# Kernel tuning notes

Hardware: AMD Instinct MI355X
Metric: run time of the kernel (lower is better)

## Reference

```python
import jax, jax.numpy as jnp
import numpy as np

B, T, N, F_DIM = 8, 32, 64, 6
D, H, C = 128, 4, 32          # hidden, spatial heads, head dim
L_SP, L_T, TH = 3, 3, 4       # spatial layers, temporal layers, temporal heads
THD = D // TH                 # temporal head dim
E = N * (N - 1)


def _ln(x, g, b, eps=1e-5):
    mu = x.mean(-1, keepdims=True)
    var = ((x - mu) ** 2).mean(-1, keepdims=True)
    return (x - mu) * jax.lax.rsqrt(var + eps) * g + b


def setup_inputs() -> dict:
    key = jax.random.key(0)
    ks = iter(jax.random.split(key, 64))
    r = lambda *s: jax.random.normal(next(ks), s, jnp.float32) * 0.05
    src_n, dst_n = np.nonzero(~np.eye(N, dtype=bool))
    inp = {
        'input_frames': jax.random.normal(next(ks), (B, T, N, F_DIM), jnp.float32),
        'edge_attr_seq': jax.random.uniform(next(ks), (B, T, E, 1), jnp.float32),
        'proj_W': r(F_DIM, D), 'proj_b': r(D),
        'sp_Wq': r(L_SP, D, D), 'sp_bq': r(L_SP, D),
        'sp_Wk': r(L_SP, D, D), 'sp_bk': r(L_SP, D),
        'sp_Wv': r(L_SP, D, D), 'sp_bv': r(L_SP, D),
        'sp_We': r(L_SP, 1, D), 'sp_be': r(L_SP, D),
        'sp_Ws': r(L_SP, D, D), 'sp_bs': r(L_SP, D),
        'sp_lng': jnp.ones((L_SP, D), jnp.float32), 'sp_lnb': jnp.zeros((L_SP, D), jnp.float32),
        'temporal_pos': r(1, 512, D),
        't_Wqkv': r(L_T, D, 3 * D), 't_bqkv': r(L_T, 3 * D),
        't_Wo': r(L_T, D, D), 't_bo': r(L_T, D),
        't_ln1g': jnp.ones((L_T, D), jnp.float32), 't_ln1b': jnp.zeros((L_T, D), jnp.float32),
        't_W1': r(L_T, D, 4 * D), 't_b1': r(L_T, 4 * D),
        't_W2': r(L_T, 4 * D, D), 't_b2': r(L_T, D),
        't_ln2g': jnp.ones((L_T, D), jnp.float32), 't_ln2b': jnp.zeros((L_T, D), jnp.float32),
        'head_W1': r(D, D), 'head_b1': r(D),
        'head_W2': r(D, F_DIM), 'head_b2': r(F_DIM),
        'edge_index': jnp.asarray(np.stack([src_n, dst_n]), jnp.int32),
    }
    return inp


def _forward(input_frames, edge_attr_seq, proj_W, proj_b, sp_Wq, sp_bq, sp_Wk, sp_bk,
             sp_Wv, sp_bv, sp_We, sp_be, sp_Ws, sp_bs, sp_lng, sp_lnb, temporal_pos,
             t_Wqkv, t_bqkv, t_Wo, t_bo, t_ln1g, t_ln1b, t_W1, t_b1, t_W2, t_b2,
             t_ln2g, t_ln2b, head_W1, head_b1, head_W2, head_b2, edge_index):
    BT = B * T
    Nt = BT * N                                       # total batched nodes
    offs = jnp.arange(BT, dtype=edge_index.dtype) * N
    src = (edge_index[0][None, :] + offs[:, None]).reshape(-1)   # (BT*E,)
    dst = (edge_index[1][None, :] + offs[:, None]).reshape(-1)
    ea = edge_attr_seq.reshape(BT * E, 1)
    h = input_frames.reshape(Nt, F_DIM) @ proj_W + proj_b        # (Nt, D)

    scale = 1.0 / jnp.sqrt(jnp.float32(C))
    for l in range(L_SP):
        q = (h @ sp_Wq[l] + sp_bq[l]).reshape(Nt, H, C)
        k = (h @ sp_Wk[l] + sp_bk[l]).reshape(Nt, H, C)
        v = (h @ sp_Wv[l] + sp_bv[l]).reshape(Nt, H, C)
        e = (ea @ sp_We[l] + sp_be[l]).reshape(-1, H, C)         # (Et, H, C)
        kj = k[src] + e
        alpha = (q[dst] * kj).sum(-1) * scale                    # (Et, H)
        amax = jax.ops.segment_max(alpha, dst, num_segments=Nt)
        ae = jnp.exp(alpha - amax[dst])
        asum = jax.ops.segment_sum(ae, dst, num_segments=Nt)
        w = ae / asum[dst]                                       # segment softmax
        msg = (v[src] + e) * w[..., None]
        agg = jax.ops.segment_sum(msg, dst, num_segments=Nt).reshape(Nt, D)
        out = agg + h @ sp_Ws[l] + sp_bs[l]                      # root/skip term
        h = _ln(h + out, sp_lng[l], sp_lnb[l])

    z = h.reshape(B, T, N, D).transpose(0, 2, 1, 3).reshape(B * N, T, D)
    z = z + temporal_pos[:, :T, :]

    causal = jnp.tril(jnp.ones((T, T), bool))
    tscale = 1.0 / jnp.sqrt(jnp.float32(THD))
    for l in range(L_T):
        qkv = z @ t_Wqkv[l] + t_bqkv[l]
        q, k, v = jnp.split(qkv, 3, axis=-1)
        q = q.reshape(B * N, T, TH, THD)
        k = k.reshape(B * N, T, TH, THD)
        v = v.reshape(B * N, T, TH, THD)
        s = jnp.einsum('bqhd,bkhd->bhqk', q, k) * tscale
        s = jnp.where(causal, s, -jnp.inf)
        a = jax.nn.softmax(s, axis=-1)
        o = jnp.einsum('bhqk,bkhd->bqhd', a, v).reshape(B * N, T, D)
        o = o @ t_Wo[l] + t_bo[l]
        z = _ln(z + o, t_ln1g[l], t_ln1b[l])
        f = jax.nn.gelu(z @ t_W1[l] + t_b1[l], approximate=False) @ t_W2[l] + t_b2[l]
        z = _ln(z + f, t_ln2g[l], t_ln2b[l])

    h_last = z[:, -1, :].reshape(B, N, D)
    pred = jax.nn.gelu(h_last @ head_W1 + head_b1, approximate=False) @ head_W2 + head_b2
    return pred                                                  # (B, N, F)


def reference(input_frames, edge_attr_seq, proj_W, proj_b, sp_Wq, sp_bq, sp_Wk, sp_bk,
              sp_Wv, sp_bv, sp_We, sp_be, sp_Ws, sp_bs, sp_lng, sp_lnb, temporal_pos,
              t_Wqkv, t_bqkv, t_Wo, t_bo, t_ln1g, t_ln1b, t_W1, t_b1, t_W2, t_b2,
              t_ln2g, t_ln2b, head_W1, head_b1, head_W2, head_b2, edge_index):
    return _forward(input_frames, edge_attr_seq, proj_W, proj_b, sp_Wq, sp_bq, sp_Wk,
                    sp_bk, sp_Wv, sp_bv, sp_We, sp_be, sp_Ws, sp_bs, sp_lng, sp_lnb,
                    temporal_pos, t_Wqkv, t_bqkv, t_Wo, t_bo, t_ln1g, t_ln1b, t_W1,
                    t_b1, t_W2, t_b2, t_ln2g, t_ln2b, head_W1, head_b1, head_W2,
                    head_b2, edge_index)
```

## Files before the change

kernel.cpp:

```cpp
#include <hip/hip_runtime.h>
#include <hip/hip_bf16.h>
#include <math.h>

typedef __hip_bfloat16 bf16;
typedef short short8 __attribute__((ext_vector_type(8)));
typedef float floatx4 __attribute__((ext_vector_type(4)));

#define B_    8
#define T_    32
#define N_    64
#define F_    6
#define D_    128
#define E_    4032
#define BT_   256
#define BN_   512

__device__ __forceinline__ float gelu_exact(float x) {
    return 0.5f * x * (1.0f + erff(x * 0.70710678118654752f));
}
__device__ __forceinline__ float bfbits2f(short s) {
    unsigned int u = ((unsigned int)(unsigned short)s) << 16;
    return __uint_as_float(u);
}
__device__ __forceinline__ void ld32lds(const bf16* p, float* o) {
    const short8* sp = (const short8*)p;
#pragma unroll
    for (int i = 0; i < 4; i++) {
        short8 s = sp[i];
#pragma unroll
        for (int j = 0; j < 8; j++) o[i * 8 + j] = bfbits2f(s[j]);
    }
}

struct RepackDesc { const float* W; bf16* out; int K, N, ntt, ntoff, L, start; };
struct RepackArgs { RepackDesc d[9]; int total; };

__global__ void k_repack(RepackArgs ra) {
    int gid = blockIdx.x * blockDim.x + threadIdx.x;
    if (gid >= ra.total) return;
    int fi = 0;
    while (fi < 8 && gid >= ra.d[fi + 1].start) fi++;
    RepackDesc dd = ra.d[fi];
    int r = gid - dd.start;
    int lane = r & 63; r >>= 6;
    int ntiles = dd.N >> 4;
    int nt = r % ntiles; r /= ntiles;
    int ktiles = dd.K >> 5;
    int kt = r % ktiles;
    int l = r / ktiles;
    int quad = lane >> 4, cc = lane & 15;
    const float* Wl = dd.W + (size_t)l * dd.K * dd.N;
    bf16* o = dd.out + ((((size_t)l * ktiles + kt) * dd.ntt + nt + dd.ntoff) * 64 + lane) * 8;
    int kb = kt * 32 + quad * 8;
    int n = nt * 16 + cc;
#pragma unroll
    for (int j = 0; j < 8; j++)
        o[j] = __float2bfloat16(Wl[(size_t)(kb + j) * dd.N + n]);
}

__global__ void k_packbias(const float* __restrict__ bq, const float* __restrict__ bk,
                           const float* __restrict__ bv, float* __restrict__ out) {
    int i = blockIdx.x * blockDim.x + threadIdx.x;
    if (i >= 3 * 384) return;
    int l = i / 384, c = i % 384;
    float v = (c < 128) ? bq[l * 128 + c]
            : (c < 256) ? bk[l * 128 + c - 128]
                        : bv[l * 128 + c - 256];
    out[i] = v;
}

__global__ __launch_bounds__(512, 1)
void k_spatial3(const float* __restrict__ inp, const float* __restrict__ projW,
                const float* __restrict__ projB,
                const short8* __restrict__ BpQKV, const short8* __restrict__ BpWS,
                const float* __restrict__ spb, const float* __restrict__ bs,
                const float* __restrict__ lng, const float* __restrict__ lnb,
                const float* __restrict__ ea, const float* __restrict__ Weg,
                const float* __restrict__ beg, const float* __restrict__ tpos,
                float* __restrict__ z32g) {
    __shared__ short smem[61312];
    bf16* hb = (bf16*)smem;
    bf16* qk = (bf16*)(smem + 8704);
    float* aggf = (float*)(smem + 8704);
    float* fsm = (float*)(smem + 8704);
    bf16* Vt = (bf16*)(smem + 25600);
    bf16* Ps = (bf16*)(smem + 34816);
    float* EAs = (float*)(smem + 53248);

    int bt = blockIdx.x;
    int tid = threadIdx.x;
    int lane = tid & 63, w = tid >> 6;
    int quad = lane >> 4, col = lane & 15;
    int w4 = w & 3, wh = w >> 2;
    const float scale = 0.17677669529663687f;

    for (int i = tid; i < 896; i += 512)
        fsm[i] = (i < 768) ? projW[i] : projB[i - 768];
    {
        const float* eag = ea + (size_t)bt * E_;
        for (int i = tid; i < E_; i += 512) EAs[i] = eag[i];
    }
    __syncthreads();
    float hreg[32];
    if (w < 4) {
#pragma unroll
        for (int r = 0; r < 4; r++) {
            int n = w * 16 + quad * 4 + r;
            const float* xr = inp + (size_t)(bt * 64 + n) * F_;
            float xin[6];
#pragma unroll
            for (int k2 = 0; k2 < 6; k2++) xin[k2] = xr[k2];
#pragma unroll
            for (int tt = 0; tt < 8; tt++) {
                int c = tt * 16 + col;
                float a = fsm[768 + c];
#pragma unroll
                for (int k2 = 0; k2 < 6; k2++) a = fmaf(xin[k2], fsm[k2 * 128 + c], a);
                hreg[tt * 4 + r] = a;
                hb[n * 136 + c] = __float2bfloat16(a);
            }
        }
    }
    __syncthreads();

    for (int l = 0; l < 3; l++) {
        {
            floatx4 acc[12];
#pragma unroll
            for (int tt = 0; tt < 12; tt++) acc[tt] = (floatx4){0.f, 0.f, 0.f, 0.f};
            const short8* bpl = BpQKV + (size_t)l * 6144;
            for (int kt = 0; kt < 4; kt++) {
                short8 a = *(const short8*)&hb[(w4 * 16 + col) * 136 + kt * 32 + quad * 8];
                const short8* bp = bpl + (size_t)(kt * 24 + wh * 12) * 64 + lane;
#pragma unroll
                for (int tt = 0; tt < 12; tt++)
                    acc[tt] = __builtin_amdgcn_mfma_f32_16x16x32_bf16(a, bp[tt * 64], acc[tt], 0, 0, 0);
            }
            const float* bias = spb + l * 384;
#pragma unroll
            for (int tt = 0; tt < 12; tt++) {
                int c = wh * 192 + tt * 16 + col;
                float bv = bias[c];
#pragma unroll
                for (int r = 0; r < 4; r++) {
                    int row = w4 * 16 + quad * 4 + r;
                    bf16 v = __float2bfloat16(acc[tt][r] + bv);
                    if (c < 256) qk[row * 264 + c] = v;
                    else         Vt[(c - 256) * 72 + row] = v;
                }
            }
        }
        __syncthreads();
        int h = w4, half = wh;
        int hoff = h * 32;
        const float* Wel = Weg + l * 128 + hoff;
        const float* bel = beg + l * 128 + hoff;
        float qWe;
        {
            int dst = half * 32 + (lane & 31);
            float qr[32];
            ld32lds(&qk[dst * 264 + hoff], qr);
            float s0 = 0.f, s1 = 0.f, s2 = 0.f, s3 = 0.f;
#pragma unroll
            for (int c2 = 0; c2 < 32; c2 += 4) {
                s0 = fmaf(qr[c2], Wel[c2], s0);
                s1 = fmaf(qr[c2 + 1], Wel[c2 + 1], s1);
                s2 = fmaf(qr[c2 + 2], Wel[c2 + 2], s2);
                s3 = fmaf(qr[c2 + 3], Wel[c2 + 3], s3);
            }
            qWe = (s0 + s1) + (s2 + s3);
        }
        float s[2][4][4], ev[2][4][4];
        {
            short8 aA[2], bB[4];
#pragma unroll
            for (int mtl = 0; mtl < 2; mtl++)
                aA[mtl] = *(const short8*)&qk[((half * 2 + mtl) * 16 + col) * 264 + hoff + quad * 8];
#pragma unroll
            for (int nt = 0; nt < 4; nt++)
                bB[nt] = *(const short8*)&qk[(nt * 16 + col) * 264 + 128 + hoff + quad * 8];
#pragma unroll
            for (int mtl = 0; mtl < 2; mtl++)
#pragma unroll
                for (int nt = 0; nt < 4; nt++) {
                    floatx4 acc = (floatx4){0.f, 0.f, 0.f, 0.f};
                    acc = __builtin_amdgcn_mfma_f32_16x16x32_bf16(aA[mtl], bB[nt], acc, 0, 0, 0);
#pragma unroll
                    for (int r = 0; r < 4; r++) s[mtl][nt][r] = acc[r];
                }
        }
        __syncthreads();
        float ls[2][4], ae[2][4], inv[2][4];
#pragma unroll
        for (int mtl = 0; mtl < 2; mtl++)
#pragma unroll
            for (int r = 0; r < 4; r++) {
                int m = half * 32 + mtl * 16 + quad * 4 + r;
                float qWeR = __shfl(qWe, mtl * 16 + quad * 4 + r, 64);
                float rmax = -1e30f;
#pragma unroll
                for (int nt = 0; nt < 4; nt++) {
                    int n = nt * 16 + col;
                    bool diag = (m == n);
                    int eid = diag ? 0 : (n * 63 + m - (m > n ? 1 : 0));
                    float eav = diag ? 0.f : EAs[eid];
                    ev[mtl][nt][r] = eav;
                    float al = diag ? -1e30f
                                    : scale * (s[mtl][nt][r] + eav * qWeR);
                    s[mtl][nt][r] = al;
                    rmax = fmaxf(rmax, al);
                }
#pragma unroll
                for (int mk2 = 1; mk2 <= 8; mk2 <<= 1)
                    rmax = fmaxf(rmax, __shfl_xor(rmax, mk2, 64));
                float lsum = 0.f, aesum = 0.f;
#pragma unroll
                for (int nt = 0; nt < 4; nt++) {
                    float p = __expf(s[mtl][nt][r] - rmax);
                    s[mtl][nt][r] = p;
                    lsum += p;
                    aesum = fmaf(p, ev[mtl][nt][r], aesum);
                }
#pragma unroll
                for (int mk2 = 1; mk2 <= 8; mk2 <<= 1) {
                    lsum += __shfl_xor(lsum, mk2, 64);
                    aesum += __shfl_xor(aesum, mk2, 64);
                }
                ls[mtl][r] = lsum;
                ae[mtl][r] = aesum;
                inv[mtl][r] = 1.0f / lsum;
            }
        bf16* PsH = Ps + h * 4608;
        floatx4 oacc[2][2];
#pragma unroll
        for (int mtl = 0; mtl < 2; mtl++)
#pragma unroll
            for (int ntB = 0; ntB < 2; ntB++) oacc[mtl][ntB] = (floatx4){0.f, 0.f, 0.f, 0.f};
#pragma unroll
        for (int p = 0; p < 2; p++) {
#pragma unroll
            for (int mtl = 0; mtl < 2; mtl++)
#pragma unroll
                for (int q2 = 0; q2 < 2; q2++) {
                    int nl = q2 * 16 + col;
                    int base0 = (half * 32 + mtl * 16 + quad * 4) * 72 + ((nl >> 3) * 2) * 8 + (nl & 7);
#pragma unroll
                    for (int r = 0; r < 4; r++) {
                        float p_ = s[mtl][2 * p + q2][r];
                        bf16 hi = __float2bfloat16(p_);
                        bf16 lo = __float2bfloat16(p_ - bfbits2f(*(short*)&hi));
                        PsH[base0 + r * 72] = hi;
                        PsH[base0 + r * 72 + 8] = lo;
                    }
                }
            short8 aPh[2], aPl[2], bV[2];
#pragma unroll
            for (int mtl = 0; mtl < 2; mtl++) {
                int rb = (half * 32 + mtl * 16 + col) * 72 + quad * 16;
                aPh[mtl] = *(const short8*)&PsH[rb];
                aPl[mtl] = *(const short8*)&PsH[rb + 8];
            }
#pragma unroll
            for (int ntB = 0; ntB < 2; ntB++)
                bV[ntB] = *(const short8*)&Vt[(hoff + ntB * 16 + col) * 72 + p * 32 + quad * 8];
#pragma unroll
            for (int mtl = 0; mtl < 2; mtl++)
#pragma unroll
                for (int ntB = 0; ntB < 2; ntB++) {
                    oacc[mtl][ntB] = __builtin_amdgcn_mfma_f32_16x16x32_bf16(aPh[mtl], bV[ntB], oacc[mtl][ntB], 0, 0, 0);
                    oacc[mtl][ntB] = __builtin_amdgcn_mfma_f32_16x16x32_bf16(aPl[mtl], bV[ntB], oacc[mtl][ntB], 0, 0, 0);
                }
        }
#pragma unroll
        for (int mtl = 0; mtl < 2; mtl++)
#pragma unroll
            for (int ntB = 0; ntB < 2; ntB++) {
                int c = hoff + ntB * 16 + col;
                float Wc = Wel[ntB * 16 + col];
                float bc = bel[ntB * 16 + col];
#pragma unroll
                for (int r = 0; r < 4; r++) {
                    int m = half * 32 + mtl * 16 + quad * 4 + r;
                    aggf[m * 128 + c] = fmaf(fmaf(ae[mtl][r], Wc, oacc[mtl][ntB][r]),
                                             inv[mtl][r], bc);
                }
            }
        __syncthreads();
        if (w < 4) {
            floatx4 acc2[8];
#pragma unroll
            for (int tt = 0; tt < 8; tt++) acc2[tt] = (floatx4){0.f, 0.f, 0.f, 0.f};
            const short8* bpl = BpWS + (size_t)l * 2048;
            for (int kt = 0; kt < 4; kt++) {
                short8 a = *(const short8*)&hb[(w * 16 + col) * 136 + kt * 32 + quad * 8];
                const short8* bp = bpl + (size_t)(kt * 8) * 64 + lane;
#pragma unroll
                for (int tt = 0; tt < 8; tt++)
                    acc2[tt] = __builtin_amdgcn_mfma_f32_16x16x32_bf16(a, bp[tt * 64], acc2[tt], 0, 0, 0);
            }
            const float* bsl = bs + l * 128;
            float vv[32], rs[4] = {0.f, 0.f, 0.f, 0.f};
#pragma unroll
            for (int tt = 0; tt < 8; tt++) {
                int c = tt * 16 + col;
                float bv = bsl[c];
#pragma unroll
                for (int r = 0; r < 4; r++) {
                    int row = w * 16 + quad * 4 + r;
                    float v = acc2[tt][r] + bv + aggf[row * 128 + c] + hreg[tt * 4 + r];
                    vv[tt * 4 + r] = v;
                    rs[r] += v;
                }
            }
#pragma unroll
            for (int m = 1; m <= 8; m <<= 1)
#pragma unroll
                for (int r = 0; r < 4; r++) rs[r] += __shfl_xor(rs[r], m, 64);
            float mean[4], vs[4] = {0.f, 0.f, 0.f, 0.f};
#pragma unroll
            for (int r = 0; r < 4; r++) mean[r] = rs[r] * (1.0f / 128.0f);
#pragma unroll
            for (int i = 0; i < 32; i++) {
                float d = vv[i] - mean[i & 3];
                vv[i] = d;
                vs[i & 3] += d * d;
            }
#pragma unroll
            for (int m = 1; m <= 8; m <<= 1)
#pragma unroll
                for (int r = 0; r < 4; r++) vs[r] += __shfl_xor(vs[r], m, 64);
            float inv2[4];
#pragma unroll
            for (int r = 0; r < 4; r++) inv2[r] = rsqrtf(vs[r] * (1.0f / 128.0f) + 1e-5f);
            const float* gl = lng + l * 128;
            const float* bl = lnb + l * 128;
            if (l < 2) {
#pragma unroll
                for (int tt = 0; tt < 8; tt++) {
                    int c = tt * 16 + col;
                    float gc = gl[c], bc = bl[c];
#pragma unroll
                    for (int r = 0; r < 4; r++) {
                        float y = vv[tt * 4 + r] * inv2[r] * gc + bc;
                        int n = w * 16 + quad * 4 + r;
                        hreg[tt * 4 + r] = y;
                        hb[n * 136 + c] = __float2bfloat16(y);
                    }
                }
            } else {
                int b = bt >> 5, t_ = bt & 31;
#pragma unroll
                for (int tt = 0; tt < 8; tt++) {
                    int c = tt * 16 + col;
                    float gc = gl[c], bc = bl[c], pc = tpos[t_ * 128 + c];
#pragma unroll
                    for (int r = 0; r < 4; r++) {
                        float y = vv[tt * 4 + r] * inv2[r] * gc + bc;
                        int n = w * 16 + quad * 4 + r;
                        z32g[((size_t)(b * 64 + n) * 32 + t_) * 128 + c] = y + pc;
                    }
                }
            }
        }
        __syncthreads();
    }
}

__global__ __launch_bounds__(256, 2)
void k_temporal3(const float* __restrict__ z32g,
                 const short8* __restrict__ BpQKV, const short8* __restrict__ BpWO,
                 const short8* __restrict__ BpW1, const short8* __restrict__ BpW2,
                 const float* __restrict__ bqkv, const float* __restrict__ bo,
                 const float* __restrict__ ln1g, const float* __restrict__ ln1b,
                 const float* __restrict__ b1, const float* __restrict__ b2,
                 const float* __restrict__ ln2g, const float* __restrict__ ln2b,
                 bf16* __restrict__ zlastb) {
    __shared__ short smem[31488];
    bf16* zb  = (bf16*)smem;
    bf16* qk  = (bf16*)(smem + 4352);
    bf16* Ps  = (bf16*)(smem + 12800);
    bf16* Vt  = (bf16*)(smem + 22016);
    bf16* o16 = (bf16*)(smem + 27136);
    bf16* f1  = (bf16*)(smem + 4352);

    int bn = blockIdx.x;
    int tid = threadIdx.x;
    int lane = tid & 63, w = tid >> 6;
    int quad = lane >> 4, col = lane & 15;
    int rsel = w & 1, csel = w >> 1;
    const float scale = 0.17677669529663687f;

    for (int i = tid; i < 4096; i += 256) {
        float v = z32g[(size_t)bn * 4096 + i];
        zb[(i >> 7) * 136 + (i & 127)] = __float2bfloat16(v);
    }
    float zreg[32];
    if (w < 2) {
#pragma unroll
        for (int tt = 0; tt < 8; tt++)
#pragma unroll
            for (int r = 0; r < 4; r++)
                zreg[tt * 4 + r] = z32g[(size_t)bn * 4096 +
                                        (w * 16 + quad * 4 + r) * 128 + tt * 16 + col];
    }
    __syncthreads();

    for (int l = 0; l < 3; l++) {
        {
            floatx4 acc[12];
#pragma unroll
            for (int tt = 0; tt < 12; tt++) acc[tt] = (floatx4){0.f, 0.f, 0.f, 0.f};
            const short8* bpl = BpQKV + (size_t)l * 6144;
            for (int kt = 0; kt < 4; kt++) {
                short8 a = *(const short8*)&zb[(rsel * 16 + col) * 136 + kt * 32 + quad * 8];
                const short8* bp = bpl + (size_t)(kt * 24 + csel * 12) * 64 + lane;
#pragma unroll
                for (int tt = 0; tt < 12; tt++)
                    acc[tt] = __builtin_amdgcn_mfma_f32_16x16x32_bf16(a, bp[tt * 64], acc[tt], 0, 0, 0);
            }
            const float* bias = bqkv + l * 384;
#pragma unroll
            for (int tt = 0; tt < 12; tt++) {
                int c = csel * 192 + tt * 16 + col;
                float bv = bias[c];
#pragma unroll
                for (int r = 0; r < 4; r++) {
                    int row = rsel * 16 + quad * 4 + r;
                    bf16 v = __float2bfloat16(acc[tt][r] + bv);
                    if (c < 256) qk[row * 264 + c] = v;
                    else         Vt[(c - 256) * 40 + row] = v;
                }
            }
        }
        __syncthreads();
        {
            int h = w, hoff = h * 32;
            bf16* PsH = Ps + h * 2304;
            float s[2][2][4];
            short8 aA[2], bB[2];
#pragma unroll
            for (int mt = 0; mt < 2; mt++)
                aA[mt] = *(const short8*)&qk[(mt * 16 + col) * 264 + hoff + quad * 8];
#pragma unroll
            for (int nt = 0; nt < 2; nt++)
                bB[nt] = *(const short8*)&qk[(nt * 16 + col) * 264 + 128 + hoff + quad * 8];
#pragma unroll
            for (int mt = 0; mt < 2; mt++)
#pragma unroll
                for (int nt = 0; nt < 2; nt++) {
                    floatx4 acc = (floatx4){0.f, 0.f, 0.f, 0.f};
                    acc = __builtin_amdgcn_mfma_f32_16x16x32_bf16(aA[mt], bB[nt], acc, 0, 0, 0);
#pragma unroll
                    for (int r = 0; r < 4; r++) s[mt][nt][r] = acc[r];
                }
            float inv[2][4];
#pragma unroll
            for (int mt = 0; mt < 2; mt++)
#pragma unroll
                for (int r = 0; r < 4; r++) {
                    int m = mt * 16 + quad * 4 + r;
                    float rmax = -1e30f;
#pragma unroll
                    for (int nt = 0; nt < 2; nt++) {
                        int n = nt * 16 + col;
                        float al = (n > m) ? -1e30f : s[mt][nt][r] * scale;
                        s[mt][nt][r] = al;
                        rmax = fmaxf(rmax, al);
                    }
#pragma unroll
                    for (int mk2 = 1; mk2 <= 8; mk2 <<= 1)
                        rmax = fmaxf(rmax, __shfl_xor(rmax, mk2, 64));
                    float lsum = 0.f;
#pragma unroll
                    for (int nt = 0; nt < 2; nt++) {
                        float p = __expf(s[mt][nt][r] - rmax);
                        s[mt][nt][r] = p;
                        lsum += p;
                    }
#pragma unroll
                    for (int mk2 = 1; mk2 <= 8; mk2 <<= 1)
                        lsum += __shfl_xor(lsum, mk2, 64);
                    inv[mt][r] = 1.0f / lsum;
                }
#pragma unroll
            for (int mt = 0; mt < 2; mt++)
#pragma unroll
                for (int nt = 0; nt < 2; nt++) {
                    int n = nt * 16 + col;
                    int base0 = (mt * 16 + quad * 4) * 72 + ((n >> 3) * 2) * 8 + (n & 7);
#pragma unroll
                    for (int r = 0; r < 4; r++) {
                        float p_ = s[mt][nt][r];
                        bf16 hi = __float2bfloat16(p_);
                        bf16 lo = __float2bfloat16(p_ - bfbits2f(*(short*)&hi));
                        PsH[base0 + r * 72] = hi;
                        PsH[base0 + r * 72 + 8] = lo;
                    }
                }
            floatx4 oacc[2][2];
#pragma unroll
            for (int mt = 0; mt < 2; mt++)
#pragma unroll
                for (int nt = 0; nt < 2; nt++) oacc[mt][nt] = (floatx4){0.f, 0.f, 0.f, 0.f};
            short8 aPh[2], aPl[2], bV[2];
#pragma unroll
            for (int mt = 0; mt < 2; mt++) {
                int rb = (mt * 16 + col) * 72 + quad * 16;
                aPh[mt] = *(const short8*)&PsH[rb];
                aPl[mt] = *(const short8*)&PsH[rb + 8];
            }
#pragma unroll
            for (int nt = 0; nt < 2; nt++)
                bV[nt] = *(const short8*)&Vt[(hoff + nt * 16 + col) * 40 + quad * 8];
#pragma unroll
            for (int mt = 0; mt < 2; mt++)
#pragma unroll
                for (int nt = 0; nt < 2; nt++) {
                    oacc[mt][nt] = __builtin_amdgcn_mfma_f32_16x16x32_bf16(aPh[mt], bV[nt], oacc[mt][nt], 0, 0, 0);
                    oacc[mt][nt] = __builtin_amdgcn_mfma_f32_16x16x32_bf16(aPl[mt], bV[nt], oacc[mt][nt], 0, 0, 0);
                }
#pragma unroll
            for (int mt = 0; mt < 2; mt++)
#pragma unroll
                for (int nt = 0; nt < 2; nt++) {
                    int c = hoff + nt * 16 + col;
#pragma unroll
                    for (int r = 0; r < 4; r++)
                        o16[(mt * 16 + quad * 4 + r) * 136 + c] =
                            __float2bfloat16(oacc[mt][nt][r] * inv[mt][r]);
                }
        }
        __syncthreads();
        if (w < 2) {
            floatx4 acc2[8];
#pragma unroll
            for (int tt = 0; tt < 8; tt++) acc2[tt] = (floatx4){0.f, 0.f, 0.f, 0.f};
            const short8* bpl = BpWO + (size_t)l * 2048;
            for (int kt = 0; kt < 4; kt++) {
                short8 a = *(const short8*)&o16[(w * 16 + col) * 136 + kt * 32 + quad * 8];
                const short8* bp = bpl + (size_t)(kt * 8) * 64 + lane;
#pragma unroll
                for (int tt = 0; tt < 8; tt++)
                    acc2[tt] = __builtin_amdgcn_mfma_f32_16x16x32_bf16(a, bp[tt * 64], acc2[tt], 0, 0, 0);
            }
            const float* bol = bo + l * 128;
            float vv[32], rs[4] = {0.f, 0.f, 0.f, 0.f};
#pragma unroll
            for (int tt = 0; tt < 8; tt++) {
                int c = tt * 16 + col;
                float bv = bol[c];
#pragma unroll
                for (int r = 0; r < 4; r++) {
                    float v = acc2[tt][r] + bv + zreg[tt * 4 + r];
                    vv[tt * 4 + r] = v;
                    rs[r] += v;
                }
            }
#pragma unroll
            for (int m = 1; m <= 8; m <<= 1)
#pragma unroll
                for (int r = 0; r < 4; r++) rs[r] += __shfl_xor(rs[r], m, 64);
            float mean[4], vs[4] = {0.f, 0.f, 0.f, 0.f};
#pragma unroll
            for (int r = 0; r < 4; r++) mean[r] = rs[r] * (1.0f / 128.0f);
#pragma unroll
            for (int i = 0; i < 32; i++) {
                float d = vv[i] - mean[i & 3];
                vv[i] = d;
                vs[i & 3] += d * d;
            }
#pragma unroll
            for (int m = 1; m <= 8; m <<= 1)
#pragma unroll
                for (int r = 0; r < 4; r++) vs[r] += __shfl_xor(vs[r], m, 64);
            float inv2[4];
#pragma unroll
            for (int r = 0; r < 4; r++) inv2[r] = rsqrtf(vs[r] * (1.0f / 128.0f) + 1e-5f);
            const float* gl = ln1g + l * 128;
            const float* bl = ln1b + l * 128;
#pragma unroll
            for (int tt = 0; tt < 8; tt++) {
                int c = tt * 16 + col;
                float gc = gl[c], bc = bl[c];
#pragma unroll
                for (int r = 0; r < 4; r++) {
                    float y = vv[tt * 4 + r] * inv2[r] * gc + bc;
                    int row = w * 16 + quad * 4 + r;
                    zreg[tt * 4 + r] = y;
                    zb[row * 136 + c] = __float2bfloat16(y);
                }
            }
        }
        __syncthreads();
        {
            floatx4 acc3[16];
#pragma unroll
            for (int tt = 0; tt < 16; tt++) acc3[tt] = (floatx4){0.f, 0.f, 0.f, 0.f};
            const short8* bpl = BpW1 + (size_t)l * 8192;
            for (int kt = 0; kt < 4; kt++) {
                short8 a = *(const short8*)&zb[(rsel * 16 + col) * 136 + kt * 32 + quad * 8];
                const short8* bp = bpl + (size_t)(kt * 32 + csel * 16) * 64 + lane;
#pragma unroll
                for (int tt = 0; tt < 16; tt++)
                    acc3[tt] = __builtin_amdgcn_mfma_f32_16x16x32_bf16(a, bp[tt * 64], acc3[tt], 0, 0, 0);
            }
            const float* b1l = b1 + l * 512;
#pragma unroll
            for (int tt = 0; tt < 16; tt++) {
                int c = csel * 256 + tt * 16 + col;
                float bv = b1l[c];
#pragma unroll
                for (int r = 0; r < 4; r++) {
                    float v = gelu_exact(acc3[tt][r] + bv);
                    f1[(rsel * 16 + quad * 4 + r) * 520 + c] = __float2bfloat16(v);
                }
            }
        }
        __syncthreads();
        if (w < 2) {
            floatx4 acc4[8];
#pragma unroll
            for (int tt = 0; tt < 8; tt++) acc4[tt] = (floatx4){0.f, 0.f, 0.f, 0.f};
            const short8* bpl = BpW2 + (size_t)l * 8192;
            for (int kt = 0; kt < 16; kt++) {
                short8 a = *(const short8*)&f1[(w * 16 + col) * 520 + kt * 32 + quad * 8];
                const short8* bp = bpl + (size_t)(kt * 8) * 64 + lane;
#pragma unroll
                for (int tt = 0; tt < 8; tt++)
                    acc4[tt] = __builtin_amdgcn_mfma_f32_16x16x32_bf16(a, bp[tt * 64], acc4[tt], 0, 0, 0);
            }
            const float* b2l = b2 + l * 128;
            float vv[32], rs[4] = {0.f, 0.f, 0.f, 0.f};
#pragma unroll
            for (int tt = 0; tt < 8; tt++) {
                int c = tt * 16 + col;
                float bv = b2l[c];
#pragma unroll
                for (int r = 0; r < 4; r++) {
                    float v = acc4[tt][r] + bv + zreg[tt * 4 + r];
                    vv[tt * 4 + r] = v;
                    rs[r] += v;
                }
            }
#pragma unroll
            for (int m = 1; m <= 8; m <<= 1)
#pragma unroll
                for (int r = 0; r < 4; r++) rs[r] += __shfl_xor(rs[r], m, 64);
            float mean[4], vs[4] = {0.f, 0.f, 0.f, 0.f};
#pragma unroll
            for (int r = 0; r < 4; r++) mean[r] = rs[r] * (1.0f / 128.0f);
#pragma unroll
            for (int i = 0; i < 32; i++) {
                float d = vv[i] - mean[i & 3];
                vv[i] = d;
                vs[i & 3] += d * d;
            }
#pragma unroll
            for (int m = 1; m <= 8; m <<= 1)
#pragma unroll
                for (int r = 0; r < 4; r++) vs[r] += __shfl_xor(vs[r], m, 64);
            float inv2[4];
#pragma unroll
            for (int r = 0; r < 4; r++) inv2[r] = rsqrtf(vs[r] * (1.0f / 128.0f) + 1e-5f);
            const float* gl = ln2g + l * 128;
            const float* bl = ln2b + l * 128;
#pragma unroll
            for (int tt = 0; tt < 8; tt++) {
                int c = tt * 16 + col;
                float gc = gl[c], bc = bl[c];
#pragma unroll
                for (int r = 0; r < 4; r++) {
                    float y = vv[tt * 4 + r] * inv2[r] * gc + bc;
                    int row = w * 16 + quad * 4 + r;
                    zreg[tt * 4 + r] = y;
                    if (l < 2) zb[row * 136 + c] = __float2bfloat16(y);
                    else if (row == 31) zlastb[(size_t)bn * 128 + c] = __float2bfloat16(y);
                }
            }
        }
        __syncthreads();
    }
}

__global__ __launch_bounds__(256)
void k_head(const bf16* __restrict__ zlastb, const short8* __restrict__ BpHW1,
            const float* __restrict__ b1, const float* __restrict__ W2,
            const float* __restrict__ b2, float* __restrict__ out) {
    __shared__ bf16 h1[64 * 136];
    int blk = blockIdx.x;
    int tid = threadIdx.x;
    int lane = tid & 63, w = tid >> 6;
    int quad = lane >> 4, col = lane & 15;
    {
        floatx4 acc[8];
#pragma unroll
        for (int tt = 0; tt < 8; tt++) acc[tt] = (floatx4){0.f, 0.f, 0.f, 0.f};
        const short8* Ap = (const short8*)(zlastb + (size_t)(blk * 64 + w * 16 + col) * 128) + quad;
        for (int kt = 0; kt < 4; kt++) {
            short8 a = Ap[kt * 4];
            const short8* bp = BpHW1 + (size_t)(kt * 8) * 64 + lane;
#pragma unroll
            for (int tt = 0; tt < 8; tt++)
                acc[tt] = __builtin_amdgcn_mfma_f32_16x16x32_bf16(a, bp[tt * 64], acc[tt], 0, 0, 0);
        }
#pragma unroll
        for (int tt = 0; tt < 8; tt++) {
            int c = tt * 16 + col;
            float bv = b1[c];
#pragma unroll
            for (int r = 0; r < 4; r++)
                h1[(w * 16 + quad * 4 + r) * 136 + c] = __float2bfloat16(gelu_exact(acc[tt][r] + bv));
        }
    }
    __syncthreads();
    for (int idx = tid; idx < 512; idx += 256) {
        int row = idx >> 3, c = idx & 7;
        if (c < 6) {
            float a0 = 0.f, a1 = 0.f, a2 = 0.f, a3 = 0.f;
            const bf16* hr = &h1[row * 136];
#pragma unroll 8
            for (int k = 0; k < 128; k += 4) {
                a0 = fmaf(bfbits2f(*(const short*)&hr[k]),     W2[k * 6 + c], a0);
                a1 = fmaf(bfbits2f(*(const short*)&hr[k + 1]), W2[(k + 1) * 6 + c], a1);
                a2 = fmaf(bfbits2f(*(const short*)&hr[k + 2]), W2[(k + 2) * 6 + c], a2);
                a3 = fmaf(bfbits2f(*(const short*)&hr[k + 3]), W2[(k + 3) * 6 + c], a3);
            }
            out[(size_t)(blk * 64 + row) * 6 + c] = (a0 + a1) + (a2 + a3) + b2[c];
        }
    }
}

extern "C" void kernel_launch(void* const* d_in, const int* in_sizes, int n_in,
                              void* d_out, int out_size, void* d_ws, size_t ws_size,
                              hipStream_t stream) {
    const float* input_frames = (const float*)d_in[0];
    const float* edge_attr    = (const float*)d_in[1];
    const float* proj_W  = (const float*)d_in[2];
    const float* proj_b  = (const float*)d_in[3];
    const float* sp_Wq   = (const float*)d_in[4];
    const float* sp_bq   = (const float*)d_in[5];
    const float* sp_Wk   = (const float*)d_in[6];
    const float* sp_bk   = (const float*)d_in[7];
    const float* sp_Wv   = (const float*)d_in[8];
    const float* sp_bv   = (const float*)d_in[9];
    const float* sp_We   = (const float*)d_in[10];
    const float* sp_be   = (const float*)d_in[11];
    const float* sp_Ws   = (const float*)d_in[12];
    const float* sp_bs   = (const float*)d_in[13];
    const float* sp_lng  = (const float*)d_in[14];
    const float* sp_lnb  = (const float*)d_in[15];
    const float* tpos    = (const float*)d_in[16];
    const float* t_Wqkv  = (const float*)d_in[17];
    const float* t_bqkv  = (const float*)d_in[18];
    const float* t_Wo    = (const float*)d_in[19];
    const float* t_bo    = (const float*)d_in[20];
    const float* t_ln1g  = (const float*)d_in[21];
    const float* t_ln1b  = (const float*)d_in[22];
    const float* t_W1    = (const float*)d_in[23];
    const float* t_b1    = (const float*)d_in[24];
    const float* t_W2    = (const float*)d_in[25];
    const float* t_b2    = (const float*)d_in[26];
    const float* t_ln2g  = (const float*)d_in[27];
    const float* t_ln2b  = (const float*)d_in[28];
    const float* head_W1 = (const float*)d_in[29];
    const float* head_b1 = (const float*)d_in[30];
    const float* head_W2 = (const float*)d_in[31];
    const float* head_b2 = (const float*)d_in[32];

    float* f     = (float*)d_ws;
    float* z32g  = f;
    bf16*  zlastb = (bf16*)(f + (1u << 21));
    float* spb   = f + (1u << 21) + 65536;
    bf16* BpBase = (bf16*)(f + (1u << 21) + 65536 + 2048);
    bf16* BpSPQKV = BpBase;
    bf16* BpWS    = BpSPQKV + 147456;
    bf16* BpTQKV  = BpWS + 49152;
    bf16* BpWO    = BpTQKV + 147456;
    bf16* BpW1    = BpWO + 49152;
    bf16* BpW2    = BpW1 + 196608;
    bf16* BpHW1   = BpW2 + 196608;

    RepackArgs ra;
    int s = 0;
    auto mk = [&](int i, const float* W, bf16* out, int K, int N, int ntt, int ntoff, int L) {
        ra.d[i] = {W, out, K, N, ntt, ntoff, L, s};
        s += L * (K >> 5) * (N >> 4) * 64;
    };
    mk(0, sp_Wq, BpSPQKV, 128, 128, 24, 0, 3);
    mk(1, sp_Wk, BpSPQKV, 128, 128, 24, 8, 3);
    mk(2, sp_Wv, BpSPQKV, 128, 128, 24, 16, 3);
    mk(3, sp_Ws, BpWS, 128, 128, 8, 0, 3);
    mk(4, t_Wqkv, BpTQKV, 128, 384, 24, 0, 3);
    mk(5, t_Wo, BpWO, 128, 128, 8, 0, 3);
    mk(6, t_W1, BpW1, 128, 512, 32, 0, 3);
    mk(7, t_W2, BpW2, 512, 128, 8, 0, 3);
    mk(8, head_W1, BpHW1, 128, 128, 8, 0, 1);
    ra.total = s;
    k_repack<<<(s + 255) / 256, 256, 0, stream>>>(ra);
    k_packbias<<<(3 * 384 + 255) / 256, 256, 0, stream>>>(sp_bq, sp_bk, sp_bv, spb);

    k_spatial3<<<BT_, 512, 0, stream>>>(
        input_frames, proj_W, proj_b,
        (const short8*)BpSPQKV, (const short8*)BpWS,
        spb, sp_bs, sp_lng, sp_lnb, edge_attr, sp_We, sp_be, tpos, z32g);

    k_temporal3<<<BN_, 256, 0, stream>>>(
        z32g, (const short8*)BpTQKV, (const short8*)BpWO,
        (const short8*)BpW1, (const short8*)BpW2,
        t_bqkv, t_bo, t_ln1g, t_ln1b, t_b1, t_b2, t_ln2g, t_ln2b, zlastb);

    k_head<<<8, 256, 0, stream>>>(zlastb, (const short8*)BpHW1, head_b1,
                                  head_W2, head_b2, (float*)d_out);
}
```

Before: 289.5 us.

## Double temporal kernel block to 512 threads and split LayerNorm across waves

The temporal transformer kernel now runs 8 waves per block instead of 4. Every wave takes a share of each GEMM's columns, where before only 2 waves did the output-projection and FFN-down GEMMs. Attention is split by head and row-half. LayerNorm now uses a single-pass sum and sum-of-squares reduction, with per-wave partials exchanged through a small shared-memory buffer plus an extra barrier. The aim is to remove idle waves and cut per-thread register pressure, at the cost of more synchronisation and slightly less numerically stable variance.

```diff
diff --git a/kernel.cpp b/kernel.cpp
--- a/kernel.cpp
+++ b/kernel.cpp
@@ -366,7 +366,7 @@
     }
 }
 
-__global__ __launch_bounds__(256, 2)
+__global__ __launch_bounds__(512, 4)
 void k_temporal3(const float* __restrict__ z32g,
                  const short8* __restrict__ BpQKV, const short8* __restrict__ BpWO,
                  const short8* __restrict__ BpW1, const short8* __restrict__ BpW2,
@@ -375,57 +375,56 @@
                  const float* __restrict__ b1, const float* __restrict__ b2,
                  const float* __restrict__ ln2g, const float* __restrict__ ln2b,
                  bf16* __restrict__ zlastb) {
-    __shared__ short smem[31488];
+    __shared__ short smem[32000];
     bf16* zb  = (bf16*)smem;
     bf16* qk  = (bf16*)(smem + 4352);
     bf16* Ps  = (bf16*)(smem + 12800);
     bf16* Vt  = (bf16*)(smem + 22016);
     bf16* o16 = (bf16*)(smem + 27136);
+    float* lnp = (float*)(smem + 31488);
     bf16* f1  = (bf16*)(smem + 4352);
 
     int bn = blockIdx.x;
     int tid = threadIdx.x;
     int lane = tid & 63, w = tid >> 6;
     int quad = lane >> 4, col = lane & 15;
-    int rsel = w & 1, csel = w >> 1;
+    int mt = w & 1, cq = w >> 1;
     const float scale = 0.17677669529663687f;
 
-    for (int i = tid; i < 4096; i += 256) {
+    for (int i = tid; i < 4096; i += 512) {
         float v = z32g[(size_t)bn * 4096 + i];
         zb[(i >> 7) * 136 + (i & 127)] = __float2bfloat16(v);
     }
-    float zreg[32];
-    if (w < 2) {
-#pragma unroll
-        for (int tt = 0; tt < 8; tt++)
-#pragma unroll
-            for (int r = 0; r < 4; r++)
-                zreg[tt * 4 + r] = z32g[(size_t)bn * 4096 +
-                                        (w * 16 + quad * 4 + r) * 128 + tt * 16 + col];
-    }
+    float zreg[8];
+#pragma unroll
+    for (int t2 = 0; t2 < 2; t2++)
+#pragma unroll
+        for (int r = 0; r < 4; r++)
+            zreg[t2 * 4 + r] = z32g[(size_t)bn * 4096 +
+                                    (mt * 16 + quad * 4 + r) * 128 + cq * 32 + t2 * 16 + col];
     __syncthreads();
 
     for (int l = 0; l < 3; l++) {
         {
-            floatx4 acc[12];
-#pragma unroll
-            for (int tt = 0; tt < 12; tt++) acc[tt] = (floatx4){0.f, 0.f, 0.f, 0.f};
+            floatx4 acc[6];
+#pragma unroll
+            for (int tt = 0; tt < 6; tt++) acc[tt] = (floatx4){0.f, 0.f, 0.f, 0.f};
             const short8* bpl = BpQKV + (size_t)l * 6144;
             for (int kt = 0; kt < 4; kt++) {
-                short8 a = *(const short8*)&zb[(rsel * 16 + col) * 136 + kt * 32 + quad * 8];
-                const short8* bp = bpl + (size_t)(kt * 24 + csel * 12) * 64 + lane;
-#pragma unroll
-                for (int tt = 0; tt < 12; tt++)
+                short8 a = *(const short8*)&zb[(mt * 16 + col) * 136 + kt * 32 + quad * 8];
+                const short8* bp = bpl + (size_t)(kt * 24 + cq * 6) * 64 + lane;
+#pragma unroll
+                for (int tt = 0; tt < 6; tt++)
                     acc[tt] = __builtin_amdgcn_mfma_f32_16x16x32_bf16(a, bp[tt * 64], acc[tt], 0, 0, 0);
             }
             const float* bias = bqkv + l * 384;
 #pragma unroll
-            for (int tt = 0; tt < 12; tt++) {
-                int c = csel * 192 + tt * 16 + col;
+            for (int tt = 0; tt < 6; tt++) {
+                int c = cq * 96 + tt * 16 + col;
                 float bv = bias[c];
 #pragma unroll
                 for (int r = 0; r < 4; r++) {
-                    int row = rsel * 16 + quad * 4 + r;
+                    int row = mt * 16 + quad * 4 + r;
                     bf16 v = __float2bfloat16(acc[tt][r] + bv);
                     if (c < 256) qk[row * 264 + c] = v;
                     else         Vt[(c - 256) * 40 + row] = v;
@@ -434,158 +433,146 @@
         }
         __syncthreads();
         {
-            int h = w, hoff = h * 32;
-            bf16* PsH = Ps + h * 2304;
-            float s[2][2][4];
-            short8 aA[2], bB[2];
-#pragma unroll
-            for (int mt = 0; mt < 2; mt++)
-                aA[mt] = *(const short8*)&qk[(mt * 16 + col) * 264 + hoff + quad * 8];
+            int h = w & 3, mh = w >> 2;
+            int hoff = h * 32;
+            bf16* PsH = Ps + (h * 2 + mh) * 1152;
+            float s[2][4];
+            short8 aA = *(const short8*)&qk[(mh * 16 + col) * 264 + hoff + quad * 8];
+            short8 bB[2];
 #pragma unroll
             for (int nt = 0; nt < 2; nt++)
                 bB[nt] = *(const short8*)&qk[(nt * 16 + col) * 264 + 128 + hoff + quad * 8];
 #pragma unroll
-            for (int mt = 0; mt < 2; mt++)
-#pragma unroll
-                for (int nt = 0; nt < 2; nt++) {
-                    floatx4 acc = (floatx4){0.f, 0.f, 0.f, 0.f};
-                    acc = __builtin_amdgcn_mfma_f32_16x16x32_bf16(aA[mt], bB[nt], acc, 0, 0, 0);
-#pragma unroll
-                    for (int r = 0; r < 4; r++) s[mt][nt][r] = acc[r];
-                }
-            float inv[2][4];
-#pragma unroll
-            for (int mt = 0; mt < 2; mt++)
-#pragma unroll
-                for (int r = 0; r < 4; r++) {
-                    int m = mt * 16 + quad * 4 + r;
-                    float rmax = -1e30f;
-#pragma unroll
-                    for (int nt = 0; nt < 2; nt++) {
-                        int n = nt * 16 + col;
-                        float al = (n > m) ? -1e30f : s[mt][nt][r] * scale;
-                        s[mt][nt][r] = al;
-                        rmax = fmaxf(rmax, al);
-                    }
-#pragma unroll
-                    for (int mk2 = 1; mk2 <= 8; mk2 <<= 1)
-                        rmax = fmaxf(rmax, __shfl_xor(rmax, mk2, 64));
-                    float lsum = 0.f;
-#pragma unroll
-                    for (int nt = 0; nt < 2; nt++) {
-                        float p = __expf(s[mt][nt][r] - rmax);
-                        s[mt][nt][r] = p;
-                        lsum += p;
-                    }
-#pragma unroll
-                    for (int mk2 = 1; mk2 <= 8; mk2 <<= 1)
-                        lsum += __shfl_xor(lsum, mk2, 64);
-                    inv[mt][r] = 1.0f / lsum;
-                }
-#pragma unroll
-            for (int mt = 0; mt < 2; mt++)
+            for (int nt = 0; nt < 2; nt++) {
+                floatx4 acc = (floatx4){0.f, 0.f, 0.f, 0.f};
+                acc = __builtin_amdgcn_mfma_f32_16x16x32_bf16(aA, bB[nt], acc, 0, 0, 0);
+#pragma unroll
+                for (int r = 0; r < 4; r++) s[nt][r] = acc[r];
+            }
+            float inv[4];
+#pragma unroll
+            for (int r = 0; r < 4; r++) {
+                int m = mh * 16 + quad * 4 + r;
+                float rmax = -1e30f;
 #pragma unroll
                 for (int nt = 0; nt < 2; nt++) {
                     int n = nt * 16 + col;
-                    int base0 = (mt * 16 + quad * 4) * 72 + ((n >> 3) * 2) * 8 + (n & 7);
-#pragma unroll
-                    for (int r = 0; r < 4; r++) {
-                        float p_ = s[mt][nt][r];
-                        bf16 hi = __float2bfloat16(p_);
-                        bf16 lo = __float2bfloat16(p_ - bfbits2f(*(short*)&hi));
-                        PsH[base0 + r * 72] = hi;
-                        PsH[base0 + r * 72 + 8] = lo;
-                    }
-                }
-            floatx4 oacc[2][2];
-#pragma unroll
-            for (int mt = 0; mt < 2; mt++)
-#pragma unroll
-                for (int nt = 0; nt < 2; nt++) oacc[mt][nt] = (floatx4){0.f, 0.f, 0.f, 0.f};
-            short8 aPh[2], aPl[2], bV[2];
-#pragma unroll
-            for (int mt = 0; mt < 2; mt++) {
-                int rb = (mt * 16 + col) * 72 + quad * 16;
-                aPh[mt] = *(const short8*)&PsH[rb];
-                aPl[mt] = *(const short8*)&PsH[rb + 8];
-            }
+                    float al = (n > m) ? -1e30f : s[nt][r] * scale;
+                    s[nt][r] = al;
+                    rmax = fmaxf(rmax, al);
+                }
+#pragma unroll
+                for (int mk2 = 1; mk2 <= 8; mk2 <<= 1)
+                    rmax = fmaxf(rmax, __shfl_xor(rmax, mk2, 64));
+                float lsum = 0.f;
+#pragma unroll
+                for (int nt = 0; nt < 2; nt++) {
+                    float p = __expf(s[nt][r] - rmax);
+                    s[nt][r] = p;
+                    lsum += p;
+                }
+#pragma unroll
+                for (int mk2 = 1; mk2 <= 8; mk2 <<= 1)
+                    lsum += __shfl_xor(lsum, mk2, 64);
+                inv[r] = 1.0f / lsum;
+            }
+#pragma unroll
+            for (int nt = 0; nt < 2; nt++) {
+                int n = nt * 16 + col;
+                int base0 = (quad * 4) * 72 + ((n >> 3) * 2) * 8 + (n & 7);
+#pragma unroll
+                for (int r = 0; r < 4; r++) {
+                    float p_ = s[nt][r];
+                    bf16 hi = __float2bfloat16(p_);
+                    bf16 lo = __float2bfloat16(p_ - bfbits2f(*(short*)&hi));
+                    PsH[base0 + r * 72] = hi;
+                    PsH[base0 + r * 72 + 8] = lo;
+                }
+            }
+            floatx4 oacc[2];
+#pragma unroll
+            for (int nt = 0; nt < 2; nt++) oacc[nt] = (floatx4){0.f, 0.f, 0.f, 0.f};
+            short8 aPh = *(const short8*)&PsH[col * 72 + quad * 16];
+            short8 aPl = *(const short8*)&PsH[col * 72 + quad * 16 + 8];
+            short8 bV[2];
 #pragma unroll
             for (int nt = 0; nt < 2; nt++)
                 bV[nt] = *(const short8*)&Vt[(hoff + nt * 16 + col) * 40 + quad * 8];
 #pragma unroll
-            for (int mt = 0; mt < 2; mt++)
-#pragma unroll
-                for (int nt = 0; nt < 2; nt++) {
-                    oacc[mt][nt] = __builtin_amdgcn_mfma_f32_16x16x32_bf16(aPh[mt], bV[nt], oacc[mt][nt], 0, 0, 0);
-                    oacc[mt][nt] = __builtin_amdgcn_mfma_f32_16x16x32_bf16(aPl[mt], bV[nt], oacc[mt][nt], 0, 0, 0);
-                }
-#pragma unroll
-            for (int mt = 0; mt < 2; mt++)
-#pragma unroll
-                for (int nt = 0; nt < 2; nt++) {
-                    int c = hoff + nt * 16 + col;
-#pragma unroll
-                    for (int r = 0; r < 4; r++)
-                        o16[(mt * 16 + quad * 4 + r) * 136 + c] =
-                            __float2bfloat16(oacc[mt][nt][r] * inv[mt][r]);
-                }
+            for (int nt = 0; nt < 2; nt++) {
+                oacc[nt] = __builtin_amdgcn_mfma_f32_16x16x32_bf16(aPh, bV[nt], oacc[nt], 0, 0, 0);
+                oacc[nt] = __builtin_amdgcn_mfma_f32_16x16x32_bf16(aPl, bV[nt], oacc[nt], 0, 0, 0);
+            }
+#pragma unroll
+            for (int nt = 0; nt < 2; nt++) {
+                int c = hoff + nt * 16 + col;
+#pragma unroll
+                for (int r = 0; r < 4; r++)
+                    o16[(mh * 16 + quad * 4 + r) * 136 + c] =
+                        __float2bfloat16(oacc[nt][r] * inv[r]);
+            }
         }
         __syncthreads();
-        if (w < 2) {
-            floatx4 acc2[8];
-#pragma unroll
-            for (int tt = 0; tt < 8; tt++) acc2[tt] = (floatx4){0.f, 0.f, 0.f, 0.f};
+        {
+            floatx4 acc2[2];
+#pragma unroll
+            for (int tt = 0; tt < 2; tt++) acc2[tt] = (floatx4){0.f, 0.f, 0.f, 0.f};
             const short8* bpl = BpWO + (size_t)l * 2048;
             for (int kt = 0; kt < 4; kt++) {
-                short8 a = *(const short8*)&o16[(w * 16 + col) * 136 + kt * 32 + quad * 8];
-                const short8* bp = bpl + (size_t)(kt * 8) * 64 + lane;
-#pragma unroll
-                for (int tt = 0; tt < 8; tt++)
+                short8 a = *(const short8*)&o16[(mt * 16 + col) * 136 + kt * 32 + quad * 8];
+                const short8* bp = bpl + (size_t)(kt * 8 + cq * 2) * 64 + lane;
+#pragma unroll
+                for (int tt = 0; tt < 2; tt++)
                     acc2[tt] = __builtin_amdgcn_mfma_f32_16x16x32_bf16(a, bp[tt * 64], acc2[tt], 0, 0, 0);
             }
             const float* bol = bo + l * 128;
-            float vv[32], rs[4] = {0.f, 0.f, 0.f, 0.f};
-#pragma unroll
-            for (int tt = 0; tt < 8; tt++) {
-                int c = tt * 16 + col;
+            float vv[8], rs[4] = {0.f, 0.f, 0.f, 0.f}, rq[4] = {0.f, 0.f, 0.f, 0.f};
+#pragma unroll
+            for (int tt = 0; tt < 2; tt++) {
+                int c = cq * 32 + tt * 16 + col;
                 float bv = bol[c];
 #pragma unroll
                 for (int r = 0; r < 4; r++) {
                     float v = acc2[tt][r] + bv + zreg[tt * 4 + r];
                     vv[tt * 4 + r] = v;
                     rs[r] += v;
+                    rq[r] = fmaf(v, v, rq[r]);
                 }
             }
 #pragma unroll
             for (int m = 1; m <= 8; m <<= 1)
 #pragma unroll
-                for (int r = 0; r < 4; r++) rs[r] += __shfl_xor(rs[r], m, 64);
-            float mean[4], vs[4] = {0.f, 0.f, 0.f, 0.f};
-#pragma unroll
-            for (int r = 0; r < 4; r++) mean[r] = rs[r] * (1.0f / 128.0f);
-#pragma unroll
-            for (int i = 0; i < 32; i++) {
-                float d = vv[i] - mean[i & 3];
-                vv[i] = d;
-                vs[i & 3] += d * d;
-            }
-#pragma unroll
-            for (int m = 1; m <= 8; m <<= 1)
-#pragma unroll
-                for (int r = 0; r < 4; r++) vs[r] += __shfl_xor(vs[r], m, 64);
-            float inv2[4];
-#pragma unroll
-            for (int r = 0; r < 4; r++) inv2[r] = rsqrtf(vs[r] * (1.0f / 128.0f) + 1e-5f);
+                for (int r = 0; r < 4; r++) {
+                    rs[r] += __shfl_xor(rs[r], m, 64);
+                    rq[r] += __shfl_xor(rq[r], m, 64);
+                }
+            if (col == 0) {
+#pragma unroll
+                for (int r = 0; r < 4; r++) {
+                    int row = mt * 16 + quad * 4 + r;
+                    lnp[(cq * 32 + row) * 2] = rs[r];
+                    lnp[(cq * 32 + row) * 2 + 1] = rq[r];
+                }
+            }
+            __syncthreads();
             const float* gl = ln1g + l * 128;
             const float* bl = ln1b + l * 128;
 #pragma unroll
-            for (int tt = 0; tt < 8; tt++) {
-                int c = tt * 16 + col;
-                float gc = gl[c], bc = bl[c];
-#pragma unroll
-                for (int r = 0; r < 4; r++) {
-                    float y = vv[tt * 4 + r] * inv2[r] * gc + bc;
-                    int row = w * 16 + quad * 4 + r;
+            for (int r = 0; r < 4; r++) {
+                int row = mt * 16 + quad * 4 + r;
+                float sm = 0.f, sq = 0.f;
+#pragma unroll
+                for (int q2 = 0; q2 < 4; q2++) {
+                    sm += lnp[(q2 * 32 + row) * 2];
+                    sq += lnp[(q2 * 32 + row) * 2 + 1];
+                }
+                float mean = sm * (1.0f / 128.0f);
+                float var = sq * (1.0f / 128.0f) - mean * mean;
+                float iv = rsqrtf(var + 1e-5f);
+#pragma unroll
+                for (int tt = 0; tt < 2; tt++) {
+                    int c = cq * 32 + tt * 16 + col;
+                    float y = (vv[tt * 4 + r] - mean) * iv * gl[c] + bl[c];
                     zreg[tt * 4 + r] = y;
                     zb[row * 136 + c] = __float2bfloat16(y);
                 }
@@ -593,85 +580,90 @@
         }
         __syncthreads();
         {
-            floatx4 acc3[16];
-#pragma unroll
-            for (int tt = 0; tt < 16; tt++) acc3[tt] = (floatx4){0.f, 0.f, 0.f, 0.f};
+            floatx4 acc3[8];
+#pragma unroll
+            for (int tt = 0; tt < 8; tt++) acc3[tt] = (floatx4){0.f, 0.f, 0.f, 0.f};
             const short8* bpl = BpW1 + (size_t)l * 8192;
             for (int kt = 0; kt < 4; kt++) {
-                short8 a = *(const short8*)&zb[(rsel * 16 + col) * 136 + kt * 32 + quad * 8];
-                const short8* bp = bpl + (size_t)(kt * 32 + csel * 16) * 64 + lane;
-#pragma unroll
-                for (int tt = 0; tt < 16; tt++)
+                short8 a = *(const short8*)&zb[(mt * 16 + col) * 136 + kt * 32 + quad * 8];
+                const short8* bp = bpl + (size_t)(kt * 32 + cq * 8) * 64 + lane;
+#pragma unroll
+                for (int tt = 0; tt < 8; tt++)
                     acc3[tt] = __builtin_amdgcn_mfma_f32_16x16x32_bf16(a, bp[tt * 64], acc3[tt], 0, 0, 0);
             }
             const float* b1l = b1 + l * 512;
 #pragma unroll
-            for (int tt = 0; tt < 16; tt++) {
-                int c = csel * 256 + tt * 16 + col;
+            for (int tt = 0; tt < 8; tt++) {
+                int c = cq * 128 + tt * 16 + col;
                 float bv = b1l[c];
 #pragma unroll
                 for (int r = 0; r < 4; r++) {
                     float v = gelu_exact(acc3[tt][r] + bv);
-                    f1[(rsel * 16 + quad * 4 + r) * 520 + c] = __float2bfloat16(v);
+                    f1[(mt * 16 + quad * 4 + r) * 520 + c] = __float2bfloat16(v);
                 }
             }
         }
         __syncthreads();
-        if (w < 2) {
-            floatx4 acc4[8];
-#pragma unroll
-            for (int tt = 0; tt < 8; tt++) acc4[tt] = (floatx4){0.f, 0.f, 0.f, 0.f};
+        {
+            floatx4 acc4[2];
+#pragma unroll
+            for (int tt = 0; tt < 2; tt++) acc4[tt] = (floatx4){0.f, 0.f, 0.f, 0.f};
             const short8* bpl = BpW2 + (size_t)l * 8192;
             for (int kt = 0; kt < 16; kt++) {
-                short8 a = *(const short8*)&f1[(w * 16 + col) * 520 + kt * 32 + quad * 8];
-                const short8* bp = bpl + (size_t)(kt * 8) * 64 + lane;
-#pragma unroll
-                for (int tt = 0; tt < 8; tt++)
+                short8 a = *(const short8*)&f1[(mt * 16 + col) * 520 + kt * 32 + quad * 8];
+                const short8* bp = bpl + (size_t)(kt * 8 + cq * 2) * 64 + lane;
+#pragma unroll
+                for (int tt = 0; tt < 2; tt++)
                     acc4[tt] = __builtin_amdgcn_mfma_f32_16x16x32_bf16(a, bp[tt * 64], acc4[tt], 0, 0, 0);
             }
             const float* b2l = b2 + l * 128;
-            float vv[32], rs[4] = {0.f, 0.f, 0.f, 0.f};
-#pragma unroll
-            for (int tt = 0; tt < 8; tt++) {
-                int c = tt * 16 + col;
+            float vv[8], rs[4] = {0.f, 0.f, 0.f, 0.f}, rq[4] = {0.f, 0.f, 0.f, 0.f};
+#pragma unroll
+            for (int tt = 0; tt < 2; tt++) {
+                int c = cq * 32 + tt * 16 + col;
                 float bv = b2l[c];
 #pragma unroll
                 for (int r = 0; r < 4; r++) {
                     float v = acc4[tt][r] + bv + zreg[tt * 4 + r];
                     vv[tt * 4 + r] = v;
                     rs[r] += v;
+                    rq[r] = fmaf(v, v, rq[r]);
                 }
             }
 #pragma unroll
             for (int m = 1; m <= 8; m <<= 1)
 #pragma unroll
-                for (int r = 0; r < 4; r++) rs[r] += __shfl_xor(rs[r], m, 64);
-            float mean[4], vs[4] = {0.f, 0.f, 0.f, 0.f};
-#pragma unroll
-            for (int r = 0; r < 4; r++) mean[r] = rs[r] * (1.0f / 128.0f);
-#pragma unroll
-            for (int i = 0; i < 32; i++) {
-                float d = vv[i] - mean[i & 3];
-                vv[i] = d;
-                vs[i & 3] += d * d;
-            }
-#pragma unroll
-            for (int m = 1; m <= 8; m <<= 1)
-#pragma unroll
-                for (int r = 0; r < 4; r++) vs[r] += __shfl_xor(vs[r], m, 64);
-            float inv2[4];
-#pragma unroll
-            for (int r = 0; r < 4; r++) inv2[r] = rsqrtf(vs[r] * (1.0f / 128.0f) + 1e-5f);
+                for (int r = 0; r < 4; r++) {
+                    rs[r] += __shfl_xor(rs[r], m, 64);
+                    rq[r] += __shfl_xor(rq[r], m, 64);
+                }
+            if (col == 0) {
+#pragma unroll
+                for (int r = 0; r < 4; r++) {
+                    int row = mt * 16 + quad * 4 + r;
+                    lnp[(cq * 32 + row) * 2] = rs[r];
+                    lnp[(cq * 32 + row) * 2 + 1] = rq[r];
+                }
+            }
+            __syncthreads();
             const float* gl = ln2g + l * 128;
             const float* bl = ln2b + l * 128;
 #pragma unroll
-            for (int tt = 0; tt < 8; tt++) {
-                int c = tt * 16 + col;
-                float gc = gl[c], bc = bl[c];
-#pragma unroll
-                for (int r = 0; r < 4; r++) {
-                    float y = vv[tt * 4 + r] * inv2[r] * gc + bc;
-                    int row = w * 16 + quad * 4 + r;
+            for (int r = 0; r < 4; r++) {
+                int row = mt * 16 + quad * 4 + r;
+                float sm = 0.f, sq = 0.f;
+#pragma unroll
+                for (int q2 = 0; q2 < 4; q2++) {
+                    sm += lnp[(q2 * 32 + row) * 2];
+                    sq += lnp[(q2 * 32 + row) * 2 + 1];
+                }
+                float mean = sm * (1.0f / 128.0f);
+                float var = sq * (1.0f / 128.0f) - mean * mean;
+                float iv = rsqrtf(var + 1e-5f);
+#pragma unroll
+                for (int tt = 0; tt < 2; tt++) {
+                    int c = cq * 32 + tt * 16 + col;
+                    float y = (vv[tt * 4 + r] - mean) * iv * gl[c] + bl[c];
                     zreg[tt * 4 + r] = y;
                     if (l < 2) zb[row * 136 + c] = __float2bfloat16(y);
                     else if (row == 31) zlastb[(size_t)bn * 128 + c] = __float2bfloat16(y);
@@ -804,7 +796,7 @@
         (const short8*)BpSPQKV, (const short8*)BpWS,
         spb, sp_bs, sp_lng, sp_lnb, edge_attr, sp_We, sp_be, tpos, z32g);
 
-    k_temporal3<<<BN_, 256, 0, stream>>>(
+    k_temporal3<<<BN_, 512, 0, stream>>>(
         z32g, (const short8*)BpTQKV, (const short8*)BpWO,
         (const short8*)BpW1, (const short8*)BpW2,
         t_bqkv, t_bo, t_ln1g, t_ln1b, t_b1, t_b2, t_ln2g, t_ln2b, zlastb);
```

After: 285.3 us. About the same (-1.5%).
